# Optimization experiments

Hardware: AMD Instinct MI355X
Metric: run time of the kernel (lower is better)

Reference implementation:

```python
import jax, jax.numpy as jnp
import numpy as np

NEG_INF = -1.0e9  # matches torch masked_fill value


def setup_inputs() -> dict:
    key = jax.random.key(0)
    k1, k2, k3, k4 = jax.random.split(key, 4)
    B, S, H = 32, 4096, 1024
    query = jax.random.normal(k1, (B, 1, H), dtype=jnp.float32)
    keys = jax.random.normal(k2, (B, S, H), dtype=jnp.float32)
    src_mask = jax.random.randint(k3, (B, S), 0, 2) == 1
    # nn.Linear weight [out,in]; y = x @ W.T
    W_query = jax.random.normal(k4, (H, H), dtype=jnp.float32) * (1.0 / np.sqrt(H))
    return {"query": query, "keys": keys, "src_mask": src_mask, "W_query": W_query}


def reference(query, keys, src_mask, W_query):
    # projected query: [B,1,H] @ W.T -> [B,1,H]
    q = jnp.einsum("bqh,oh->bqo", query, W_query)
    # scores: [B,S] (single query squeezed)
    scores = jnp.einsum("bqh,bsh->bqs", q, keys)[:, 0, :]
    scores = jnp.where(src_mask, NEG_INF, scores)
    weights = jax.nn.softmax(scores, axis=-1)[:, None, :]  # [B,1,S]
    context = jnp.einsum("bqs,bsh->bqh", weights, keys)    # [B,1,H]
    return (context, weights)
```

## Files before the change

kernel.cpp:

```cpp
#include <hip/hip_runtime.h>
#include <math.h>

#define BB 32
#define SS 4096
#define HH 1024
#define NCHUNK 64
#define CHUNK (SS / NCHUNK)
#define NSPLIT 4
#define NEG_INF9 (-1.0e9f)

__device__ __forceinline__ float dpp_allreduce_add(float x) {
    int t;
    t = __builtin_amdgcn_update_dpp(0, __float_as_int(x), 0x111, 0xf, 0xf, false);
    x += __int_as_float(t);
    t = __builtin_amdgcn_update_dpp(0, __float_as_int(x), 0x112, 0xf, 0xf, false);
    x += __int_as_float(t);
    t = __builtin_amdgcn_update_dpp(0, __float_as_int(x), 0x114, 0xf, 0xf, false);
    x += __int_as_float(t);
    t = __builtin_amdgcn_update_dpp(0, __float_as_int(x), 0x118, 0xf, 0xf, false);
    x += __int_as_float(t);
    t = __builtin_amdgcn_update_dpp(0, __float_as_int(x), 0x142, 0xf, 0xf, false);
    x += __int_as_float(t);
    t = __builtin_amdgcn_update_dpp(0, __float_as_int(x), 0x143, 0xf, 0xf, false);
    x += __int_as_float(t);
    return __int_as_float(__builtin_amdgcn_readlane(__float_as_int(x), 63));
}

__global__ __launch_bounds__(256) void qproj_kernel(const float* __restrict__ query,
                                                    const float* __restrict__ W,
                                                    float* __restrict__ q) {
    const int b    = blockIdx.y;
    const int wave = threadIdx.x >> 6;
    const int lane = threadIdx.x & 63;

    const float4* qp = (const float4*)(query + (size_t)b * HH);
    float4 qv[4];
#pragma unroll
    for (int r = 0; r < 4; ++r) qv[r] = qp[r * 64 + lane];

    const int obase = blockIdx.x * 64 + wave * 16;
    for (int i = 0; i < 16; ++i) {
        const int o = obase + i;
        const float4* wp = (const float4*)(W + (size_t)o * HH);
        float acc = 0.f;
#pragma unroll
        for (int r = 0; r < 4; ++r) {
            const float4 wv = wp[r * 64 + lane];
            acc += wv.x * qv[r].x + wv.y * qv[r].y + wv.z * qv[r].z + wv.w * qv[r].w;
        }
        const float s = dpp_allreduce_add(acc);
        if (lane == 0) q[(size_t)b * HH + o] = s;
    }
}

__global__ __launch_bounds__(256) void attn_chunk_kernel(const float* __restrict__ q,
                                                         const float* __restrict__ keys,
                                                         const int* __restrict__ mask,
                                                         float* __restrict__ raw_scores,
                                                         float* __restrict__ pm,
                                                         float* __restrict__ pl,
                                                         float* __restrict__ pO) {
    const int b    = blockIdx.y;
    const int c    = blockIdx.x;
    const int wave = threadIdx.x >> 6;
    const int lane = threadIdx.x & 63;

    const float4* qp = (const float4*)(q + (size_t)b * HH);
    float4 qv[4];
#pragma unroll
    for (int r = 0; r < 4; ++r) qv[r] = qp[r * 64 + lane];

    const size_t bbase = (size_t)b * SS;
    const int s0 = c * CHUNK + wave * 2;
    const float4* kbase = (const float4*)(keys + (bbase + s0) * HH) + lane;

    float4 ka[2][4], kb[2][4];
    int2   mk[2];

    {
        const float4* p0 = kbase;
        const float4* p1 = kbase + 256;
#pragma unroll
        for (int r = 0; r < 4; ++r) { ka[0][r] = p0[r * 64]; kb[0][r] = p1[r * 64]; }
        mk[0] = *(const int2*)(mask + bbase + s0);
    }

    float m = -INFINITY;
    float l = 0.f;
    float4 acc[4];
#pragma unroll
    for (int r = 0; r < 4; ++r) acc[r] = make_float4(0.f, 0.f, 0.f, 0.f);

#pragma unroll
    for (int i = 0; i < CHUNK / 8; ++i) {
        const int cur = i & 1, nxt = cur ^ 1;
        if (i + 1 < CHUNK / 8) {
            const float4* p0 = kbase + (size_t)(i + 1) * 8 * 256;
            const float4* p1 = p0 + 256;
#pragma unroll
            for (int r = 0; r < 4; ++r) { ka[nxt][r] = p0[r * 64]; kb[nxt][r] = p1[r * 64]; }
            mk[nxt] = *(const int2*)(mask + bbase + s0 + 8 * (i + 1));
        }

        float x0 = 0.f, x1 = 0.f;
#pragma unroll
        for (int r = 0; r < 4; ++r) {
            x0 += ka[cur][r].x * qv[r].x + ka[cur][r].y * qv[r].y + ka[cur][r].z * qv[r].z + ka[cur][r].w * qv[r].w;
            x1 += kb[cur][r].x * qv[r].x + kb[cur][r].y * qv[r].y + kb[cur][r].z * qv[r].z + kb[cur][r].w * qv[r].w;
        }
        float sc0 = dpp_allreduce_add(x0);
        float sc1 = dpp_allreduce_add(x1);

        const int mx = __builtin_amdgcn_readfirstlane(mk[cur].x);
        const int my = __builtin_amdgcn_readfirstlane(mk[cur].y);
        if (mx != 0) sc0 = NEG_INF9;
        if (my != 0) sc1 = NEG_INF9;
        if (lane == 0) *(float2*)(raw_scores + bbase + s0 + 8 * i) = make_float2(sc0, sc1);

        const float mnew = fmaxf(m, fmaxf(sc0, sc1));
        if (mnew > m) {
            const float scale = __expf(m - mnew);
            l *= scale;
#pragma unroll
            for (int r = 0; r < 4; ++r) {
                acc[r].x *= scale; acc[r].y *= scale; acc[r].z *= scale; acc[r].w *= scale;
            }
            m = mnew;
        }
        const float p0 = __expf(sc0 - m);
        const float p1 = __expf(sc1 - m);
        l += p0 + p1;
#pragma unroll
        for (int r = 0; r < 4; ++r) {
            acc[r].x += p0 * ka[cur][r].x + p1 * kb[cur][r].x;
            acc[r].y += p0 * ka[cur][r].y + p1 * kb[cur][r].y;
            acc[r].z += p0 * ka[cur][r].z + p1 * kb[cur][r].z;
            acc[r].w += p0 * ka[cur][r].w + p1 * kb[cur][r].w;
        }
    }

    __shared__ float  sm[4];
    __shared__ float  sl[4];
    __shared__ float4 sO[4][256];
#pragma unroll
    for (int r = 0; r < 4; ++r) sO[wave][r * 64 + lane] = acc[r];
    if (lane == 0) { sm[wave] = m; sl[wave] = l; }
    __syncthreads();

    const float M = fmaxf(fmaxf(sm[0], sm[1]), fmaxf(sm[2], sm[3]));
    float f[4];
#pragma unroll
    for (int w = 0; w < 4; ++w) f[w] = __expf(sm[w] - M);
    const float L = sl[0] * f[0] + sl[1] * f[1] + sl[2] * f[2] + sl[3] * f[3];

    const int tid = threadIdx.x;
    float4 o = make_float4(0.f, 0.f, 0.f, 0.f);
#pragma unroll
    for (int w = 0; w < 4; ++w) {
        const float4 v = sO[w][tid];
        o.x += f[w] * v.x; o.y += f[w] * v.y; o.z += f[w] * v.z; o.w += f[w] * v.w;
    }
    ((float4*)(pO + ((size_t)b * NCHUNK + c) * HH))[tid] = o;
    if (tid == 0) { pm[b * NCHUNK + c] = M; pl[b * NCHUNK + c] = L; }
}

__global__ __launch_bounds__(256) void combine_kernel(const float* __restrict__ pm,
                                                      const float* __restrict__ pl,
                                                      const float* __restrict__ pO,
                                                      float* __restrict__ context,
                                                      float* __restrict__ weights) {
    const int b    = blockIdx.y;
    const int part = blockIdx.x;
    const int tid  = threadIdx.x;

    float M = -INFINITY;
#pragma unroll 8
    for (int cc = 0; cc < NCHUNK; ++cc) M = fmaxf(M, pm[b * NCHUNK + cc]);
    float L = 0.f;
#pragma unroll 8
    for (int cc = 0; cc < NCHUNK; ++cc) L += pl[b * NCHUNK + cc] * __expf(pm[b * NCHUNK + cc] - M);
    const float invL = 1.f / L;

    const int h = part * 256 + tid;
    float o = 0.f;
#pragma unroll 8
    for (int cc = 0; cc < NCHUNK; ++cc)
        o += __expf(pm[b * NCHUNK + cc] - M) * pO[((size_t)b * NCHUNK + cc) * HH + h];
    context[(size_t)b * HH + h] = o * invL;

    const int sbeg = part * (SS / NSPLIT);
    for (int s = sbeg + tid; s < sbeg + SS / NSPLIT; s += 256) {
        const float sc = weights[(size_t)b * SS + s];
        weights[(size_t)b * SS + s] = __expf(sc - M) * invL;
    }
}

extern "C" void kernel_launch(void* const* d_in, const int* in_sizes, int n_in,
                              void* d_out, int out_size, void* d_ws, size_t ws_size,
                              hipStream_t stream) {
    const float* query = (const float*)d_in[0];
    const float* keys  = (const float*)d_in[1];
    const int*   mask  = (const int*)d_in[2];
    const float* W     = (const float*)d_in[3];

    float* context = (float*)d_out;
    float* weights = (float*)d_out + (size_t)BB * HH;

    float* q  = (float*)d_ws;
    float* pm = q + (size_t)BB * HH;
    float* pl = pm + BB * NCHUNK;
    float* pO = pl + BB * NCHUNK;

    qproj_kernel<<<dim3(HH / 64, BB), 256, 0, stream>>>(query, W, q);
    attn_chunk_kernel<<<dim3(NCHUNK, BB), 256, 0, stream>>>(q, keys, mask, weights, pm, pl, pO);
    combine_kernel<<<dim3(NSPLIT, BB), 256, 0, stream>>>(pm, pl, pO, context, weights);
}
```

Before: 704.8 us.

## Stage keys via LDS async loads and fuse combine with last-block reduction

```diff
diff --git a/kernel.cpp b/kernel.cpp
--- a/kernel.cpp
+++ b/kernel.cpp
@@ -6,7 +6,8 @@
 #define HH 1024
 #define NCHUNK 64
 #define CHUNK (SS / NCHUNK)
-#define NSPLIT 4
+#define TILE 4
+#define NT (CHUNK / TILE)
 #define NEG_INF9 (-1.0e9f)
 
 __device__ __forceinline__ float dpp_allreduce_add(float x) {
@@ -26,9 +27,17 @@
     return __int_as_float(__builtin_amdgcn_readlane(__float_as_int(x), 63));
 }
 
+__device__ __forceinline__ void gload_lds16(const float* g, void* l) {
+    __builtin_amdgcn_global_load_lds((const __attribute__((address_space(1))) void*)g,
+                                     (__attribute__((address_space(3))) void*)l, 16, 0, 0);
+}
+
 __global__ __launch_bounds__(256) void qproj_kernel(const float* __restrict__ query,
                                                     const float* __restrict__ W,
-                                                    float* __restrict__ q) {
+                                                    float* __restrict__ q,
+                                                    int* __restrict__ done_cnt) {
+    if (blockIdx.x == 0 && blockIdx.y == 0 && threadIdx.x < BB) done_cnt[threadIdx.x] = 0;
+
     const int b    = blockIdx.y;
     const int wave = threadIdx.x >> 6;
     const int lane = threadIdx.x & 63;
@@ -53,37 +62,46 @@
     }
 }
 
-__global__ __launch_bounds__(256) void attn_chunk_kernel(const float* __restrict__ q,
-                                                         const float* __restrict__ keys,
-                                                         const int* __restrict__ mask,
-                                                         float* __restrict__ raw_scores,
-                                                         float* __restrict__ pm,
-                                                         float* __restrict__ pl,
-                                                         float* __restrict__ pO) {
+__global__ __launch_bounds__(256, 4) void attn_fused_kernel(const float* __restrict__ q,
+                                                            const float* __restrict__ keys,
+                                                            const int* __restrict__ mask,
+                                                            float* __restrict__ weights,
+                                                            float* __restrict__ pm,
+                                                            float* __restrict__ pl,
+                                                            float* __restrict__ pO,
+                                                            int* __restrict__ done_cnt,
+                                                            float* __restrict__ context) {
     const int b    = blockIdx.y;
     const int c    = blockIdx.x;
-    const int wave = threadIdx.x >> 6;
-    const int lane = threadIdx.x & 63;
+    const int tid  = threadIdx.x;
+    const int wave = tid >> 6;
+    const int lane = tid & 63;
+
+    __shared__ __align__(16) char kv_raw[2][TILE * HH * 4];
+    __shared__ float sscores[CHUNK];
+    __shared__ int   smask[CHUNK];
+    __shared__ float sm[4], sl[4];
+    __shared__ int   s_last;
 
     const float4* qp = (const float4*)(q + (size_t)b * HH);
     float4 qv[4];
 #pragma unroll
     for (int r = 0; r < 4; ++r) qv[r] = qp[r * 64 + lane];
 
-    const size_t bbase = (size_t)b * SS;
-    const int s0 = c * CHUNK + wave * 2;
-    const float4* kbase = (const float4*)(keys + (bbase + s0) * HH) + lane;
-
-    float4 ka[2][4], kb[2][4];
-    int2   mk[2];
-
-    {
-        const float4* p0 = kbase;
-        const float4* p1 = kbase + 256;
-#pragma unroll
-        for (int r = 0; r < 4; ++r) { ka[0][r] = p0[r * 64]; kb[0][r] = p1[r * 64]; }
-        mk[0] = *(const int2*)(mask + bbase + s0);
-    }
+    if (tid < CHUNK) smask[tid] = mask[(size_t)b * SS + c * CHUNK + tid];
+
+    const float* kchunk = keys + ((size_t)b * SS + (size_t)c * CHUNK) * HH;
+
+#define STAGE_TILE(tt, dst)                                                   \
+    {                                                                         \
+        const float* gbase = kchunk + (size_t)(tt) * TILE * HH;               \
+        _Pragma("unroll") for (int j = 0; j < 4; ++j) {                       \
+            const int p = j * 4 + wave;                                       \
+            gload_lds16(gbase + p * 256 + lane * 4, (char*)(dst) + p * 1024); \
+        }                                                                     \
+    }
+
+    STAGE_TILE(0, kv_raw[0]);
 
     float m = -INFINITY;
     float l = 0.f;
@@ -92,58 +110,49 @@
     for (int r = 0; r < 4; ++r) acc[r] = make_float4(0.f, 0.f, 0.f, 0.f);
 
 #pragma unroll
-    for (int i = 0; i < CHUNK / 8; ++i) {
-        const int cur = i & 1, nxt = cur ^ 1;
-        if (i + 1 < CHUNK / 8) {
-            const float4* p0 = kbase + (size_t)(i + 1) * 8 * 256;
-            const float4* p1 = p0 + 256;
-#pragma unroll
-            for (int r = 0; r < 4; ++r) { ka[nxt][r] = p0[r * 64]; kb[nxt][r] = p1[r * 64]; }
-            mk[nxt] = *(const int2*)(mask + bbase + s0 + 8 * (i + 1));
-        }
-
-        float x0 = 0.f, x1 = 0.f;
-#pragma unroll
-        for (int r = 0; r < 4; ++r) {
-            x0 += ka[cur][r].x * qv[r].x + ka[cur][r].y * qv[r].y + ka[cur][r].z * qv[r].z + ka[cur][r].w * qv[r].w;
-            x1 += kb[cur][r].x * qv[r].x + kb[cur][r].y * qv[r].y + kb[cur][r].z * qv[r].z + kb[cur][r].w * qv[r].w;
-        }
-        float sc0 = dpp_allreduce_add(x0);
-        float sc1 = dpp_allreduce_add(x1);
-
-        const int mx = __builtin_amdgcn_readfirstlane(mk[cur].x);
-        const int my = __builtin_amdgcn_readfirstlane(mk[cur].y);
-        if (mx != 0) sc0 = NEG_INF9;
-        if (my != 0) sc1 = NEG_INF9;
-        if (lane == 0) *(float2*)(raw_scores + bbase + s0 + 8 * i) = make_float2(sc0, sc1);
-
-        const float mnew = fmaxf(m, fmaxf(sc0, sc1));
-        if (mnew > m) {
-            const float scale = __expf(m - mnew);
+    for (int t = 0; t < NT; ++t) {
+        __syncthreads();
+        if (t + 1 < NT) STAGE_TILE(t + 1, kv_raw[(t + 1) & 1]);
+
+        const float4* kt = (const float4*)kv_raw[t & 1];
+        float4 kva[4];
+#pragma unroll
+        for (int r = 0; r < 4; ++r) kva[r] = kt[wave * 256 + r * 64 + lane];
+
+        float x = 0.f;
+#pragma unroll
+        for (int r = 0; r < 4; ++r)
+            x += kva[r].x * qv[r].x + kva[r].y * qv[r].y + kva[r].z * qv[r].z + kva[r].w * qv[r].w;
+        float sc = dpp_allreduce_add(x);
+
+        const int rr = t * TILE + wave;
+        if (smask[rr] != 0) sc = NEG_INF9;
+        if (lane == 0) sscores[rr] = sc;
+
+        if (sc > m) {
+            const float scale = __expf(m - sc);
             l *= scale;
 #pragma unroll
             for (int r = 0; r < 4; ++r) {
                 acc[r].x *= scale; acc[r].y *= scale; acc[r].z *= scale; acc[r].w *= scale;
             }
-            m = mnew;
+            m = sc;
         }
-        const float p0 = __expf(sc0 - m);
-        const float p1 = __expf(sc1 - m);
-        l += p0 + p1;
+        const float p = __expf(sc - m);
+        l += p;
 #pragma unroll
         for (int r = 0; r < 4; ++r) {
-            acc[r].x += p0 * ka[cur][r].x + p1 * kb[cur][r].x;
-            acc[r].y += p0 * ka[cur][r].y + p1 * kb[cur][r].y;
-            acc[r].z += p0 * ka[cur][r].z + p1 * kb[cur][r].z;
-            acc[r].w += p0 * ka[cur][r].w + p1 * kb[cur][r].w;
+            acc[r].x += p * kva[r].x;
+            acc[r].y += p * kva[r].y;
+            acc[r].z += p * kva[r].z;
+            acc[r].w += p * kva[r].w;
         }
     }
 
-    __shared__ float  sm[4];
-    __shared__ float  sl[4];
-    __shared__ float4 sO[4][256];
-#pragma unroll
-    for (int r = 0; r < 4; ++r) sO[wave][r * 64 + lane] = acc[r];
+    __syncthreads();
+    float4* sO = (float4*)kv_raw[0];
+#pragma unroll
+    for (int r = 0; r < 4; ++r) sO[wave * 256 + r * 64 + lane] = acc[r];
     if (lane == 0) { sm[wave] = m; sl[wave] = l; }
     __syncthreads();
 
@@ -153,45 +162,50 @@
     for (int w = 0; w < 4; ++w) f[w] = __expf(sm[w] - M);
     const float L = sl[0] * f[0] + sl[1] * f[1] + sl[2] * f[2] + sl[3] * f[3];
 
-    const int tid = threadIdx.x;
     float4 o = make_float4(0.f, 0.f, 0.f, 0.f);
 #pragma unroll
     for (int w = 0; w < 4; ++w) {
-        const float4 v = sO[w][tid];
+        const float4 v = sO[w * 256 + tid];
         o.x += f[w] * v.x; o.y += f[w] * v.y; o.z += f[w] * v.z; o.w += f[w] * v.w;
     }
     ((float4*)(pO + ((size_t)b * NCHUNK + c) * HH))[tid] = o;
     if (tid == 0) { pm[b * NCHUNK + c] = M; pl[b * NCHUNK + c] = L; }
-}
-
-__global__ __launch_bounds__(256) void combine_kernel(const float* __restrict__ pm,
-                                                      const float* __restrict__ pl,
-                                                      const float* __restrict__ pO,
-                                                      float* __restrict__ context,
-                                                      float* __restrict__ weights) {
-    const int b    = blockIdx.y;
-    const int part = blockIdx.x;
-    const int tid  = threadIdx.x;
-
-    float M = -INFINITY;
+    if (tid < CHUNK / 4) {
+        float4 s4 = make_float4(sscores[tid * 4], sscores[tid * 4 + 1],
+                                sscores[tid * 4 + 2], sscores[tid * 4 + 3]);
+        ((float4*)(weights + (size_t)b * SS + (size_t)c * CHUNK))[tid] = s4;
+    }
+
+    __threadfence();
+    __syncthreads();
+    if (tid == 0) s_last = (atomicAdd(&done_cnt[b], 1) == NCHUNK - 1);
+    __syncthreads();
+    if (!s_last) return;
+    __threadfence();
+
+    float Mb = -INFINITY;
 #pragma unroll 8
-    for (int cc = 0; cc < NCHUNK; ++cc) M = fmaxf(M, pm[b * NCHUNK + cc]);
-    float L = 0.f;
+    for (int cc = 0; cc < NCHUNK; ++cc) Mb = fmaxf(Mb, pm[b * NCHUNK + cc]);
+    float Lb = 0.f;
 #pragma unroll 8
-    for (int cc = 0; cc < NCHUNK; ++cc) L += pl[b * NCHUNK + cc] * __expf(pm[b * NCHUNK + cc] - M);
-    const float invL = 1.f / L;
-
-    const int h = part * 256 + tid;
-    float o = 0.f;
+    for (int cc = 0; cc < NCHUNK; ++cc) Lb += pl[b * NCHUNK + cc] * __expf(pm[b * NCHUNK + cc] - Mb);
+    const float invL = 1.f / Lb;
+
+    const float4* pO4 = (const float4*)pO;
+    float4 o2 = make_float4(0.f, 0.f, 0.f, 0.f);
 #pragma unroll 8
-    for (int cc = 0; cc < NCHUNK; ++cc)
-        o += __expf(pm[b * NCHUNK + cc] - M) * pO[((size_t)b * NCHUNK + cc) * HH + h];
-    context[(size_t)b * HH + h] = o * invL;
-
-    const int sbeg = part * (SS / NSPLIT);
-    for (int s = sbeg + tid; s < sbeg + SS / NSPLIT; s += 256) {
-        const float sc = weights[(size_t)b * SS + s];
-        weights[(size_t)b * SS + s] = __expf(sc - M) * invL;
+    for (int cc = 0; cc < NCHUNK; ++cc) {
+        const float g = __expf(pm[b * NCHUNK + cc] - Mb) * invL;
+        const float4 v = pO4[((size_t)b * NCHUNK + cc) * (HH / 4) + tid];
+        o2.x += g * v.x; o2.y += g * v.y; o2.z += g * v.z; o2.w += g * v.w;
+    }
+    ((float4*)(context + (size_t)b * HH))[tid] = o2;
+
+#pragma unroll
+    for (int k = 0; k < SS / 256; ++k) {
+        const size_t idx = (size_t)b * SS + k * 256 + tid;
+        const float sc = weights[idx];
+        weights[idx] = __expf(sc - Mb) * invL;
     }
 }
 
@@ -206,12 +220,13 @@
     float* context = (float*)d_out;
     float* weights = (float*)d_out + (size_t)BB * HH;
 
-    float* q  = (float*)d_ws;
-    float* pm = q + (size_t)BB * HH;
-    float* pl = pm + BB * NCHUNK;
-    float* pO = pl + BB * NCHUNK;
-
-    qproj_kernel<<<dim3(HH / 64, BB), 256, 0, stream>>>(query, W, q);
-    attn_chunk_kernel<<<dim3(NCHUNK, BB), 256, 0, stream>>>(q, keys, mask, weights, pm, pl, pO);
-    combine_kernel<<<dim3(NSPLIT, BB), 256, 0, stream>>>(pm, pl, pO, context, weights);
-}
+    float* q    = (float*)d_ws;
+    float* pm   = q + (size_t)BB * HH;
+    float* pl   = pm + BB * NCHUNK;
+    float* pO   = pl + BB * NCHUNK;
+    int*   done = (int*)(pO + (size_t)BB * NCHUNK * HH);
+
+    qproj_kernel<<<dim3(HH / 64, BB), 256, 0, stream>>>(query, W, q, done);
+    attn_fused_kernel<<<dim3(NCHUNK, BB), 256, 0, stream>>>(q, keys, mask, weights, pm, pl, pO,
+                                                            done, context);
+}
```

Result: slower. 1.069 ms (+51.7%).
